# Kernel optimization log

Hardware: AMD Instinct MI355X
Metric: run time of the kernel (lower is better)

Reference implementation:

```python
import jax, jax.numpy as jnp
import numpy as np

B, S, D = 2, 2048, 1024
H, DH, DL, DR = 16, 64, 512, 64
DHID, N_SHARED, N_ROUTED, TOPK = 512, 2, 8, 2
EPS = 1e-6


def setup_inputs() -> dict:
    key = jax.random.key(0)
    ks = jax.random.split(key, 16)
    w = lambda k, shp: jax.random.normal(k, shp, dtype=jnp.float32) * 0.02
    return {
        "x": jax.random.normal(ks[0], (B, S, D), dtype=jnp.float32),
        "mask": jnp.tril(jnp.ones((S, S), dtype=bool)),  # causal
        "w_q": w(ks[1], (D, H * (DH + DR))),
        "w_dkv": w(ks[2], (D, DL)),
        "w_uk": w(ks[3], (DL, H * DH)),
        "w_uv": w(ks[4], (DL, H * DH)),
        "w_kr": w(ks[5], (D, DR)),
        "w_o": w(ks[6], (H * DH, D)),
        "attn_norm_w": jnp.ones((D,), jnp.float32),
        "mlp_norm_w": jnp.ones((D,), jnp.float32),
        "gate_w": w(ks[7], (D, N_ROUTED)),
        "wr_gate": w(ks[8], (N_ROUTED, D, DHID)),
        "wr_up": w(ks[9], (N_ROUTED, D, DHID)),
        "wr_down": w(ks[10], (N_ROUTED, DHID, D)),
        "ws_gate": w(ks[11], (N_SHARED, D, DHID)),
        "ws_up": w(ks[12], (N_SHARED, D, DHID)),
        "ws_down": w(ks[13], (N_SHARED, DHID, D)),
    }


def _rmsnorm(x, w):
    x32 = x.astype(jnp.float32)
    n = x32 * jax.lax.rsqrt(jnp.mean(x32 * x32, axis=-1, keepdims=True) + EPS)
    return n.astype(x.dtype) * w


def _rope_tables(seq_len, dim):
    half = dim // 2
    inv = 1.0 / (10000.0 ** (jnp.arange(half, dtype=jnp.float32) / half))
    ang = jnp.arange(seq_len, dtype=jnp.float32)[:, None] * inv[None, :]  # [S, dim/2]
    return jnp.cos(ang), jnp.sin(ang)


def _rope(t, cos, sin):
    # t: [..., S, dim]; rotate-half convention
    t1, t2 = jnp.split(t, 2, axis=-1)
    return jnp.concatenate([t1 * cos - t2 * sin, t2 * cos + t1 * sin], axis=-1)


def _layer(x, mask, w_q, w_dkv, w_uk, w_uv, w_kr, w_o, attn_norm_w, mlp_norm_w,
           gate_w, wr_gate, wr_up, wr_down, ws_gate, ws_up, ws_down):
    # ---- pre-norm MLA attention + residual ----
    h = _rmsnorm(x, attn_norm_w)
    cos, sin = _rope_tables(S, DR)

    q = (h @ w_q).reshape(B, S, H, DH + DR).transpose(0, 2, 1, 3)  # [B,H,S,DH+DR]
    q_c, q_r = q[..., :DH], _rope(q[..., DH:], cos, sin)

    latent = h @ w_dkv                                              # [B,S,DL]
    k_c = (latent @ w_uk).reshape(B, S, H, DH).transpose(0, 2, 1, 3)  # [B,H,S,DH]
    v = (latent @ w_uv).reshape(B, S, H, DH).transpose(0, 2, 1, 3)
    k_r = _rope(h @ w_kr, cos, sin)                                 # [B,S,DR] shared across heads

    scale = 1.0 / np.sqrt(DH + DR)
    scores = (jnp.einsum("bhqd,bhkd->bhqk", q_c, k_c)
              + jnp.einsum("bhqd,bkd->bhqk", q_r, k_r)) * scale
    scores = jnp.where(mask, scores, jnp.float32(-1e9))
    attn = jax.nn.softmax(scores, axis=-1)
    ctx = jnp.einsum("bhqk,bhkd->bhqd", attn, v)                    # [B,H,S,DH]
    attn_out = ctx.transpose(0, 2, 1, 3).reshape(B, S, H * DH) @ w_o
    x = x + attn_out

    # ---- pre-norm shared + routed MoE FFN + residual ----
    h = _rmsnorm(x, mlp_norm_w).reshape(-1, D)                      # [T,D]
    probs = jax.nn.softmax(h @ gate_w, axis=-1)                     # [T,NR]
    vals, idx = jax.lax.top_k(probs, TOPK)                          # [T,K]
    gw = vals / jnp.sum(vals, axis=-1, keepdims=True)
    dense_w = jnp.sum(jax.nn.one_hot(idx, N_ROUTED, dtype=h.dtype) * gw[..., None], axis=1)  # [T,NR]

    g = jax.nn.silu(jnp.einsum("td,edh->teh", h, wr_gate))
    u = jnp.einsum("td,edh->teh", h, wr_up)
    y = jnp.einsum("teh,ehd->ted", g * u, wr_down)                  # [T,NR,D]
    routed = jnp.einsum("ted,te->td", y, dense_w)

    gs = jax.nn.silu(jnp.einsum("td,sdh->tsh", h, ws_gate))
    us = jnp.einsum("td,sdh->tsh", h, ws_up)
    shared = jnp.einsum("tsh,shd->td", gs * us, ws_down)

    return x + (routed + shared).reshape(B, S, D)


def reference(x, mask, w_q, w_dkv, w_uk, w_uv, w_kr, w_o, attn_norm_w, mlp_norm_w,
              gate_w, wr_gate, wr_up, wr_down, ws_gate, ws_up, ws_down):
    return _layer(x, mask, w_q, w_dkv, w_uk, w_uv, w_kr, w_o, attn_norm_w, mlp_norm_w,
                  gate_w, wr_gate, wr_up, wr_down, ws_gate, ws_up, ws_down)
```

## Files before the change

### kernel.cpp

```cpp
#include <hip/hip_runtime.h>
#include <hip/hip_bf16.h>
#include <stdint.h>

typedef unsigned short u16;
typedef __attribute__((ext_vector_type(8))) short short8;
typedef __attribute__((ext_vector_type(4))) float f32x4;
typedef __attribute__((ext_vector_type(4))) int i32x4;
typedef __attribute__((ext_vector_type(2))) unsigned int u32x2;

#define B_    2
#define S_    2048
#define D_    1024
#define H_    16
#define T_    (B_*S_)

static __device__ __forceinline__ float b2f(u16 h) { return __uint_as_float(((uint32_t)h) << 16); }
static __device__ __forceinline__ u16 f2b(float f) {
    uint32_t u = __float_as_uint(f);
    u += 0x7fffu + ((u >> 16) & 1u);
    return (u16)(u >> 16);
}
static __device__ __forceinline__ uint32_t pack2(float a, float b) {
    return (uint32_t)f2b(a) | ((uint32_t)f2b(b) << 16);
}
static __device__ __forceinline__ uint32_t cvtpk(float a, float b) {
    uint32_t r;
    asm("v_cvt_pk_bf16_f32 %0, %1, %2" : "=v"(r) : "v"(a), "v"(b));
    return r;
}
#define MFMA(a,b,c) __builtin_amdgcn_mfma_f32_16x16x32_bf16(a,b,c,0,0,0)

static __device__ __forceinline__ void gl2lds16(const void* g, void* l) {
    __builtin_amdgcn_global_load_lds((const __attribute__((address_space(1))) void*)g,
                                     (__attribute__((address_space(3))) void*)l, 16, 0, 0);
}

__global__ __launch_bounds__(256) void transpose_cvt(const float* __restrict__ in,
    u16* __restrict__ out, int K, int N, long inEZ, long outEZ)
{
    __shared__ float tile[32][33];
    const int e = blockIdx.z;
    const float* ip = in + (long)e * inEZ;
    u16* op = out + (long)e * outEZ;
    int n0 = blockIdx.x * 32, k0 = blockIdx.y * 32;
    int tx = threadIdx.x, ty = threadIdx.y;
#pragma unroll
    for (int i = 0; i < 4; ++i) {
        int k = k0 + ty + 8 * i, n = n0 + tx;
        tile[ty + 8 * i][tx] = (k < K && n < N) ? ip[(long)k * N + n] : 0.f;
    }
    __syncthreads();
#pragma unroll
    for (int i = 0; i < 4; ++i) {
        int n = n0 + ty + 8 * i, k = k0 + tx;
        if (n < N && k < K) op[(long)n * K + k] = f2b(tile[tx][ty + 8 * i]);
    }
}

__global__ __launch_bounds__(256) void gemm_k(const u16* __restrict__ A, long lda,
    const u16* __restrict__ Bt, long ldb, void* __restrict__ Cv, long ldc, int K,
    int mode, const float* __restrict__ resid)
{
    __shared__ u16 As[3][128 * 32];
    __shared__ u16 Bs[3][128 * 32];
    const int tid = threadIdx.x, lane = tid & 63, wave = tid >> 6;
    const int wm = (wave & 1) * 64, wn = (wave >> 1) * 64;
    const int quad = lane >> 4, rr = lane & 15, q8 = quad * 8;
    const long row0 = (long)blockIdx.y * 128, col0 = (long)blockIdx.x * 128;
    f32x4 acc[4][4];
#pragma unroll
    for (int i = 0; i < 4; ++i)
#pragma unroll
        for (int j = 0; j < 4; ++j)
#pragma unroll
            for (int c = 0; c < 4; ++c) acc[i][j][c] = 0.f;
    const int band = wave * 32;
    const u16* ga = A + (row0 + band + (lane >> 2)) * lda + (lane & 3) * 8;
    const u16* gb = Bt + (col0 + band + (lane >> 2)) * ldb + (lane & 3) * 8;
    const int lo = band * 32;
    const int nt = K >> 5;
#define STG(bi, k0s) do { \
    gl2lds16(ga + (k0s), &As[bi][lo]); \
    gl2lds16(ga + (k0s) + 16 * lda, &As[bi][lo + 512]); \
    gl2lds16(gb + (k0s), &Bs[bi][lo]); \
    gl2lds16(gb + (k0s) + 16 * ldb, &Bs[bi][lo + 512]); } while (0)
    STG(0, 0);
    STG(1, 32);
    asm volatile("s_waitcnt vmcnt(4)" ::: "memory");
    __builtin_amdgcn_s_barrier();
    int cur = 0, nx2 = 2;
    for (int t = 0; t < nt; ++t) {
        const bool more = (t + 2 < nt);
        if (more) STG(nx2, (t + 2) * 32);
        short8 af[4], bf[4];
#pragma unroll
        for (int mi = 0; mi < 4; ++mi) af[mi] = *(const short8*)&As[cur][(wm + mi * 16 + rr) * 32 + q8];
#pragma unroll
        for (int ni = 0; ni < 4; ++ni) bf[ni] = *(const short8*)&Bs[cur][(wn + ni * 16 + rr) * 32 + q8];
#pragma unroll
        for (int mi = 0; mi < 4; ++mi)
#pragma unroll
            for (int ni = 0; ni < 4; ++ni)
                acc[mi][ni] = MFMA(af[mi], bf[ni], acc[mi][ni]);
        if (more) asm volatile("s_waitcnt vmcnt(4)" ::: "memory");
        else      asm volatile("s_waitcnt vmcnt(0)" ::: "memory");
        __builtin_amdgcn_s_barrier();
        cur = (cur == 2) ? 0 : cur + 1;
        nx2 = (nx2 == 2) ? 0 : nx2 + 1;
    }
#undef STG
#pragma unroll
    for (int mi = 0; mi < 4; ++mi)
#pragma unroll
        for (int ni = 0; ni < 4; ++ni)
#pragma unroll
            for (int rg = 0; rg < 4; ++rg) {
                long r = row0 + wm + mi * 16 + quad * 4 + rg;
                long c = col0 + wn + ni * 16 + rr;
                float v = acc[mi][ni][rg];
                if (mode == 1)      ((u16*)Cv)[r * ldc + c] = f2b(v);
                else if (mode == 2) ((float*)Cv)[r * ldc + c] += v;
                else                ((float*)Cv)[r * ldc + c] = v + resid[r * 1024 + c];
            }
}

__global__ __launch_bounds__(256) void gemm_shdown(const u16* __restrict__ A,
    const u16* __restrict__ BtBase, float* __restrict__ Cv)
{
    __shared__ u16 As[3][128 * 32];
    __shared__ u16 Bs[3][128 * 32];
    const int tid = threadIdx.x, lane = tid & 63, wave = tid >> 6;
    const int wm = (wave & 1) * 64, wn = (wave >> 1) * 64;
    const int quad = lane >> 4, rr = lane & 15, q8 = quad * 8;
    const long row0 = (long)blockIdx.y * 128, col0 = (long)blockIdx.x * 128;
    f32x4 acc[4][4];
#pragma unroll
    for (int i = 0; i < 4; ++i)
#pragma unroll
        for (int j = 0; j < 4; ++j)
#pragma unroll
            for (int c = 0; c < 4; ++c) acc[i][j][c] = 0.f;
    const int band = wave * 32;
    const long arow = row0 + band + (lane >> 2);
    const long brow = col0 + band + (lane >> 2);
    const int lo = band * 32;
#define STG(bi, k0s) do { \
    const long aoff = ((k0s) < 512) ? (long)(k0s) : (long)(512 + (k0s)); \
    const long boff = ((k0s) < 512) ? (long)(k0s) : (long)(524288 - 512 + (k0s)); \
    const u16* ga = A + arow * 2048 + aoff + (lane & 3) * 8; \
    const u16* gb = BtBase + brow * 512 + boff + (lane & 3) * 8; \
    gl2lds16(ga, &As[bi][lo]); \
    gl2lds16(ga + 16 * 2048, &As[bi][lo + 512]); \
    gl2lds16(gb, &Bs[bi][lo]); \
    gl2lds16(gb + 16 * 512, &Bs[bi][lo + 512]); } while (0)
    const int nt = 32;
    STG(0, 0);
    STG(1, 32);
    asm volatile("s_waitcnt vmcnt(4)" ::: "memory");
    __builtin_amdgcn_s_barrier();
    int cur = 0, nx2 = 2;
    for (int t = 0; t < nt; ++t) {
        const bool more = (t + 2 < nt);
        if (more) STG(nx2, (t + 2) * 32);
        short8 af[4], bf[4];
#pragma unroll
        for (int mi = 0; mi < 4; ++mi) af[mi] = *(const short8*)&As[cur][(wm + mi * 16 + rr) * 32 + q8];
#pragma unroll
        for (int ni = 0; ni < 4; ++ni) bf[ni] = *(const short8*)&Bs[cur][(wn + ni * 16 + rr) * 32 + q8];
#pragma unroll
        for (int mi = 0; mi < 4; ++mi)
#pragma unroll
            for (int ni = 0; ni < 4; ++ni)
                acc[mi][ni] = MFMA(af[mi], bf[ni], acc[mi][ni]);
        if (more) asm volatile("s_waitcnt vmcnt(4)" ::: "memory");
        else      asm volatile("s_waitcnt vmcnt(0)" ::: "memory");
        __builtin_amdgcn_s_barrier();
        cur = (cur == 2) ? 0 : cur + 1;
        nx2 = (nx2 == 2) ? 0 : nx2 + 1;
    }
#undef STG
#pragma unroll
    for (int mi = 0; mi < 4; ++mi)
#pragma unroll
        for (int ni = 0; ni < 4; ++ni)
#pragma unroll
            for (int rg = 0; rg < 4; ++rg) {
                long r = row0 + wm + mi * 16 + quad * 4 + rg;
                long c = col0 + wn + ni * 16 + rr;
                Cv[r * 1024 + c] += acc[mi][ni][rg];
            }
}

__global__ __launch_bounds__(256) void gemm_gather(const u16* __restrict__ H2,
    const u16* __restrict__ BtAll, u16* __restrict__ C,
    const int* __restrict__ cnt, const int* __restrict__ off,
    const int* __restrict__ elist)
{
    const int e = blockIdx.z;
    const int cntE = cnt[e], offE = off[e];
    const int m0 = blockIdx.y * 128;
    if (m0 >= cntE) return;
    const u16* Bt = BtAll + (long)e * 1024 * 1024;
    __shared__ u16 As[3][128 * 32];
    __shared__ u16 Bs[3][128 * 32];
    const int tid = threadIdx.x, lane = tid & 63, wave = tid >> 6;
    const int wm = (wave & 1) * 64, wn = (wave >> 1) * 64;
    const int quad = lane >> 4, rr = lane & 15, q8 = quad * 8;
    const long col0 = (long)blockIdx.x * 128;
    f32x4 acc[4][4];
#pragma unroll
    for (int i = 0; i < 4; ++i)
#pragma unroll
        for (int j = 0; j < 4; ++j)
#pragma unroll
            for (int c = 0; c < 4; ++c) acc[i][j][c] = 0.f;
    const int band = wave * 32;
    int r0 = m0 + band + (lane >> 2);
    int r1 = r0 + 16;
    int tok0 = elist[offE + (r0 < cntE ? r0 : cntE - 1)];
    int tok1 = elist[offE + (r1 < cntE ? r1 : cntE - 1)];
    const u16* ga0 = H2 + (long)tok0 * 1024 + (lane & 3) * 8;
    const u16* ga1 = H2 + (long)tok1 * 1024 + (lane & 3) * 8;
    const u16* gb = Bt + (col0 + band + (lane >> 2)) * 1024L + (lane & 3) * 8;
    const int lo = band * 32;
#define STG(bi, k0s) do { \
    gl2lds16(ga0 + (k0s), &As[bi][lo]); \
    gl2lds16(ga1 + (k0s), &As[bi][lo + 512]); \
    gl2lds16(gb + (k0s), &Bs[bi][lo]); \
    gl2lds16(gb + (k0s) + 16 * 1024, &Bs[bi][lo + 512]); } while (0)
    const int nt = 32;
    STG(0, 0);
    STG(1, 32);
    asm volatile("s_waitcnt vmcnt(4)" ::: "memory");
    __builtin_amdgcn_s_barrier();
    int cur = 0, nx2 = 2;
    for (int t = 0; t < nt; ++t) {
        const bool more = (t + 2 < nt);
        if (more) STG(nx2, (t + 2) * 32);
        short8 af[4], bf[4];
#pragma unroll
        for (int mi = 0; mi < 4; ++mi) af[mi] = *(const short8*)&As[cur][(wm + mi * 16 + rr) * 32 + q8];
#pragma unroll
        for (int ni = 0; ni < 4; ++ni) bf[ni] = *(const short8*)&Bs[cur][(wn + ni * 16 + rr) * 32 + q8];
#pragma unroll
        for (int mi = 0; mi < 4; ++mi)
#pragma unroll
            for (int ni = 0; ni < 4; ++ni)
                acc[mi][ni] = MFMA(af[mi], bf[ni], acc[mi][ni]);
        if (more) asm volatile("s_waitcnt vmcnt(4)" ::: "memory");
        else      asm volatile("s_waitcnt vmcnt(0)" ::: "memory");
        __builtin_amdgcn_s_barrier();
        cur = (cur == 2) ? 0 : cur + 1;
        nx2 = (nx2 == 2) ? 0 : nx2 + 1;
    }
#undef STG
#pragma unroll
    for (int mi = 0; mi < 4; ++mi)
#pragma unroll
        for (int ni = 0; ni < 4; ++ni)
#pragma unroll
            for (int rg = 0; rg < 4; ++rg) {
                int ml = wm + mi * 16 + quad * 4 + rg;
                long c = col0 + wn + ni * 16 + rr;
                if (m0 + ml < cntE)
                    C[(long)(offE + m0 + ml) * 1024 + c] = f2b(acc[mi][ni][rg]);
            }
}

__global__ __launch_bounds__(256) void gemm_slot(const u16* __restrict__ Act,
    const u16* __restrict__ BtAll, u16* __restrict__ rout,
    const int* __restrict__ cnt, const int* __restrict__ off)
{
    const int e = blockIdx.z;
    const int cntE = cnt[e], offE = off[e];
    const int m0 = blockIdx.y * 128;
    if (m0 >= cntE) return;
    const u16* Bt = BtAll + (long)e * 1024 * 512;
    __shared__ u16 As[3][128 * 32];
    __shared__ u16 Bs[3][128 * 32];
    const int tid = threadIdx.x, lane = tid & 63, wave = tid >> 6;
    const int wm = (wave & 1) * 64, wn = (wave >> 1) * 64;
    const int quad = lane >> 4, rr = lane & 15, q8 = quad * 8;
    const long col0 = (long)blockIdx.x * 128;
    f32x4 acc[4][4];
#pragma unroll
    for (int i = 0; i < 4; ++i)
#pragma unroll
        for (int j = 0; j < 4; ++j)
#pragma unroll
            for (int c = 0; c < 4; ++c) acc[i][j][c] = 0.f;
    const int band = wave * 32;
    int r0 = offE + m0 + band + (lane >> 2); if (r0 > 8191) r0 = 8191;
    int r1 = r0 + 16; if (r1 > 8191) r1 = 8191;
    const u16* ga0 = Act + (long)r0 * 1024 + (lane & 3) * 8;
    const u16* ga1 = Act + (long)r1 * 1024 + (lane & 3) * 8;
    const u16* gb = Bt + (col0 + band + (lane >> 2)) * 512L + (lane & 3) * 8;
    const int lo = band * 32;
#define STG(bi, k0s) do { \
    gl2lds16(ga0 + (k0s), &As[bi][lo]); \
    gl2lds16(ga1 + (k0s), &As[bi][lo + 512]); \
    gl2lds16(gb + (k0s), &Bs[bi][lo]); \
    gl2lds16(gb + (k0s) + 16 * 512, &Bs[bi][lo + 512]); } while (0)
    const int nt = 16;
    STG(0, 0);
    STG(1, 32);
    asm volatile("s_waitcnt vmcnt(4)" ::: "memory");
    __builtin_amdgcn_s_barrier();
    int cur = 0, nx2 = 2;
    for (int t = 0; t < nt; ++t) {
        const bool more = (t + 2 < nt);
        if (more) STG(nx2, (t + 2) * 32);
        short8 af[4], bf[4];
#pragma unroll
        for (int mi = 0; mi < 4; ++mi) af[mi] = *(const short8*)&As[cur][(wm + mi * 16 + rr) * 32 + q8];
#pragma unroll
        for (int ni = 0; ni < 4; ++ni) bf[ni] = *(const short8*)&Bs[cur][(wn + ni * 16 + rr) * 32 + q8];
#pragma unroll
        for (int mi = 0; mi < 4; ++mi)
#pragma unroll
            for (int ni = 0; ni < 4; ++ni)
                acc[mi][ni] = MFMA(af[mi], bf[ni], acc[mi][ni]);
        if (more) asm volatile("s_waitcnt vmcnt(4)" ::: "memory");
        else      asm volatile("s_waitcnt vmcnt(0)" ::: "memory");
        __builtin_amdgcn_s_barrier();
        cur = (cur == 2) ? 0 : cur + 1;
        nx2 = (nx2 == 2) ? 0 : nx2 + 1;
    }
#undef STG
#pragma unroll
    for (int mi = 0; mi < 4; ++mi)
#pragma unroll
        for (int ni = 0; ni < 4; ++ni)
#pragma unroll
            for (int rg = 0; rg < 4; ++rg) {
                int ml = wm + mi * 16 + quad * 4 + rg;
                long c = col0 + wn + ni * 16 + rr;
                if (m0 + ml < cntE)
                    rout[(long)(offE + m0 + ml) * 1024 + c] = f2b(acc[mi][ni][rg]);
            }
}

__global__ __launch_bounds__(256) void rmsnorm_wave(const float* __restrict__ x,
    const float* __restrict__ w, u16* __restrict__ out)
{
    const int t = blockIdx.x * 4 + (threadIdx.x >> 6);
    const int lane = threadIdx.x & 63;
    const float* xp = x + (size_t)t * D_;
    f32x4 v[4];
    float s = 0.f;
#pragma unroll
    for (int i = 0; i < 4; ++i) {
        v[i] = *(const f32x4*)&xp[lane * 4 + i * 256];
#pragma unroll
        for (int j = 0; j < 4; ++j) s += v[i][j] * v[i][j];
    }
#pragma unroll
    for (int o = 32; o > 0; o >>= 1) s += __shfl_xor(s, o);
    const float inv = rsqrtf(s * (1.f / D_) + 1e-6f);
    u16* op = out + (size_t)t * D_;
#pragma unroll
    for (int i = 0; i < 4; ++i) {
        const int d = lane * 4 + i * 256;
        f32x4 wv = *(const f32x4*)&w[d];
        u32x2 pk;
        pk[0] = pack2(v[i][0] * inv * wv[0], v[i][1] * inv * wv[1]);
        pk[1] = pack2(v[i][2] * inv * wv[2], v[i][3] * inv * wv[3]);
        *(u32x2*)&op[d] = pk;
    }
}

__global__ __launch_bounds__(256) void rmsnorm_gate_fused(const float* __restrict__ xm,
    const float* __restrict__ nw, const float* __restrict__ gw, u16* __restrict__ h2,
    int* __restrict__ tok_e, float* __restrict__ tok_w)
{
    const int t = blockIdx.x * 4 + (threadIdx.x >> 6);
    const int lane = threadIdx.x & 63;
    const float* xp = xm + (size_t)t * D_;
    f32x4 v[4];
    float s = 0.f;
#pragma unroll
    for (int i = 0; i < 4; ++i) {
        v[i] = *(const f32x4*)&xp[lane * 4 + i * 256];
#pragma unroll
        for (int j = 0; j < 4; ++j) s += v[i][j] * v[i][j];
    }
#pragma unroll
    for (int o = 32; o > 0; o >>= 1) s += __shfl_xor(s, o);
    const float inv = rsqrtf(s * (1.f / D_) + 1e-6f);
    u16* op = h2 + (size_t)t * D_;
    float part[8] = {0,0,0,0,0,0,0,0};
#pragma unroll
    for (int i = 0; i < 4; ++i) {
        const int d = lane * 4 + i * 256;
        f32x4 wv = *(const f32x4*)&nw[d];
        float hv[4];
#pragma unroll
        for (int j = 0; j < 4; ++j) hv[j] = v[i][j] * inv * wv[j];
        u32x2 pk;
        pk[0] = pack2(hv[0], hv[1]);
        pk[1] = pack2(hv[2], hv[3]);
        *(u32x2*)&op[d] = pk;
#pragma unroll
        for (int j = 0; j < 4; ++j) {
            const float* gp = gw + (size_t)(d + j) * 8;
#pragma unroll
            for (int e = 0; e < 8; ++e) part[e] += hv[j] * gp[e];
        }
    }
#pragma unroll
    for (int e = 0; e < 8; ++e)
#pragma unroll
        for (int o = 32; o > 0; o >>= 1) part[e] += __shfl_xor(part[e], o);
    if (lane == 0) {
        float mx = part[0];
#pragma unroll
        for (int e = 1; e < 8; ++e) mx = fmaxf(mx, part[e]);
        float p[8];
#pragma unroll
        for (int e = 0; e < 8; ++e) p[e] = __expf(part[e] - mx);
        int i0 = 0;
#pragma unroll
        for (int e = 1; e < 8; ++e) if (p[e] > p[i0]) i0 = e;
        int i1 = (i0 == 0) ? 1 : 0;
#pragma unroll
        for (int e = 0; e < 8; ++e) { if (e == i0) continue; if (p[e] > p[i1]) i1 = e; }
        float sw = p[i0] + p[i1];
        tok_e[2 * t] = i0;  tok_e[2 * t + 1] = i1;
        tok_w[2 * t] = p[i0] / sw;  tok_w[2 * t + 1] = p[i1] / sw;
    }
}

__global__ __launch_bounds__(256) void moe_route(const int* __restrict__ tok_e,
    int* __restrict__ cnt, int* __restrict__ off,
    int* __restrict__ elist, int* __restrict__ tslot)
{
    const int E = blockIdx.x;
    const int tid = threadIdx.x, lane = tid & 63, wave = tid >> 6;
    int ev[32];
#pragma unroll
    for (int i = 0; i < 8; ++i)
        *(i32x4*)&ev[i * 4] = *(const i32x4*)&tok_e[tid * 32 + i * 4];
    int c8[8] = {0,0,0,0,0,0,0,0};
#pragma unroll
    for (int k = 0; k < 32; ++k) ++c8[ev[k] & 7];
    int incl[8];
#pragma unroll
    for (int e = 0; e < 8; ++e) {
        int vv = c8[e];
#pragma unroll
        for (int d = 1; d < 64; d <<= 1) {
            int tmp = __shfl_up(vv, d);
            if (lane >= d) vv += tmp;
        }
        incl[e] = vv;
    }
    __shared__ int wtot[4][8];
    if (lane == 63)
#pragma unroll
        for (int e = 0; e < 8; ++e) wtot[wave][e] = incl[e];
    __syncthreads();
    int tot[8];
#pragma unroll
    for (int e = 0; e < 8; ++e) tot[e] = wtot[0][e] + wtot[1][e] + wtot[2][e] + wtot[3][e];
    int waveoff = 0;
    for (int w = 0; w < 4; ++w) if (w < wave) waveoff += wtot[w][E];
    int offE = 0;
#pragma unroll
    for (int e = 0; e < 8; ++e) if (e < E) offE += tot[e];
    int rank = offE + waveoff + (incl[E] - c8[E]);
#pragma unroll
    for (int k = 0; k < 32; ++k) {
        if ((ev[k] & 7) == E) {
            int p = tid * 32 + k;
            elist[rank] = p >> 1;
            tslot[p] = rank;
            ++rank;
        }
    }
    if (tid == 0) { cnt[E] = tot[E]; off[E] = offE; }
}

__global__ __launch_bounds__(256) void rope_all(u16* __restrict__ proj)
{
    int idx = blockIdx.x * 256 + threadIdx.x;
    int i = idx & 31;
    int r = idx >> 5;
    int t = r / 17, which = r - t * 17;
    int s = t & (S_ - 1);
    float inv = __expf(-(float)i * 0.28782313662425575f);
    float ang = (float)s * inv;
    float c = cosf(ang), sn = sinf(ang);
    u16* base = proj + (size_t)t * 2688 + (which < 16 ? which * 128 + 64 : 2560);
    float t1 = b2f(base[i]), t2 = b2f(base[32 + i]);
    base[i]      = f2b(t1 * c - t2 * sn);
    base[32 + i] = f2b(t2 * c + t1 * sn);
}

__global__ __launch_bounds__(256, 4) void attn_flash(const u16* __restrict__ proj,
    const u16* __restrict__ kc, const u16* __restrict__ vt, u16* __restrict__ ctx)
{
    const int qidx = blockIdx.x >> 5;
    const int qt = (qidx < 8) ? (31 - qidx) : (qidx < 16) ? (qidx - 8)
                 : (qidx < 24) ? (39 - qidx) : (qidx - 16);
    const int bh = blockIdx.x & 31;
    const int b = bh >> 4, h = bh & 15;
    const int q0 = qt * 64;
    const int tid = threadIdx.x, lane = tid & 63, wave = tid >> 6;
    const int quad = lane >> 4, rr = lane & 15, q8 = quad * 8;
    const int wm2 = wave * 16;

    __shared__ u16 Ks[64 * 128];
    __shared__ u16 Ps[64 * 64];

    const long tbase = (long)b * S_ + q0;
    short8 qf[4];
#pragma unroll
    for (int d0 = 0; d0 < 4; ++d0)
        qf[d0] = *(const short8*)&proj[(tbase + wm2 + rr) * 2688 + h * 128 + d0 * 32 + q8];

    f32x4 accO[4];
    float m_i = -3e38f, l_i = 0.f;
#pragma unroll
    for (int vi = 0; vi < 4; ++vi)
#pragma unroll
        for (int rg = 0; rg < 4; ++rg) accO[vi][rg] = 0.f;
    const float sc = 0.08838834764831845f * 1.4426950408889634f;

    const int srow0 = tid >> 3, sg = tid & 7;
    const int swz = sg ^ (srow0 & 7);
    const u16* kcp = kc   + ((long)b * S_ + srow0) * 1024 + h * 64 + sg * 8;
    const u16* krp = proj + ((long)b * S_ + srow0) * 2688 + 2560 + sg * 8;
    const u16* vbase = vt + (size_t)(h * 64 + rr) * 4096 + b * 2048 + q8;
    const int rg7 = rr & 7;
    int rdcol[4];
#pragma unroll
    for (int d0 = 0; d0 < 4; ++d0) rdcol[d0] = ((d0 * 4 + quad) ^ rg7) * 8;
    const int prcol0 = (((quad * 16) ^ (rg7 << 4)) >> 1);
    const int prcol1 = (((64 + quad * 16) ^ (rg7 << 4)) >> 1);

    const int nkt = qt + 1;
    short8 rk0 = *(const short8*)(kcp);
    short8 rk1 = *(const short8*)(kcp + 32 * 1024);
    short8 rm0 = *(const short8*)(krp);
    short8 rm1 = *(const short8*)(krp + (size_t)32 * 2688);

    for (int kt = 0; kt < nkt; ++kt) {
        const int k0 = kt * 64;
        *(short8*)&Ks[srow0 * 128 + swz * 8]             = rk0;
        *(short8*)&Ks[(srow0 + 32) * 128 + swz * 8]      = rk1;
        *(short8*)&Ks[srow0 * 128 + 64 + swz * 8]        = rm0;
        *(short8*)&Ks[(srow0 + 32) * 128 + 64 + swz * 8] = rm1;
        __syncthreads();

        const size_t k0s = (kt + 1 < nkt) ? (size_t)(k0 + 64) : 0;
        short8 nk0 = *(const short8*)(kcp + k0s * 1024);
        short8 nk1 = *(const short8*)(kcp + k0s * 1024 + 32 * 1024);
        short8 nm0 = *(const short8*)(krp + k0s * 2688);
        short8 nm1 = *(const short8*)(krp + k0s * 2688 + (size_t)32 * 2688);

        f32x4 accS[4];
#pragma unroll
        for (int ki = 0; ki < 4; ++ki)
#pragma unroll
            for (int rg = 0; rg < 4; ++rg) accS[ki][rg] = 0.f;
        __builtin_amdgcn_s_setprio(1);
#pragma unroll
        for (int d0 = 0; d0 < 4; ++d0) {
            short8 kf[4];
#pragma unroll
            for (int ki = 0; ki < 4; ++ki) kf[ki] = *(const short8*)&Ks[(ki * 16 + rr) * 128 + rdcol[d0]];
#pragma unroll
            for (int ki = 0; ki < 4; ++ki) accS[ki] = MFMA(kf[ki], qf[d0], accS[ki]);
        }
        __builtin_amdgcn_s_setprio(0);
        __syncthreads();

        short8 vf0[4], vf1[4];
#pragma unroll
        for (int vi = 0; vi < 4; ++vi) {
            vf0[vi] = *(const short8*)(vbase + (size_t)vi * 16 * 4096 + k0);
            vf1[vi] = *(const short8*)(vbase + (size_t)vi * 16 * 4096 + k0 + 32);
        }

        float mx = -3e38f;
        if (kt == qt) {
            const int qg = q0 + wm2 + rr;
#pragma unroll
            for (int ki = 0; ki < 4; ++ki)
#pragma unroll
                for (int rg = 0; rg < 4; ++rg) {
                    float w = accS[ki][rg] * sc;
                    if (k0 + ki * 16 + quad * 4 + rg > qg) w = -1e30f;
                    accS[ki][rg] = w;
                    mx = fmaxf(mx, w);
                }
        } else {
#pragma unroll
            for (int ki = 0; ki < 4; ++ki)
#pragma unroll
                for (int rg = 0; rg < 4; ++rg) {
                    float w = accS[ki][rg] * sc;
                    accS[ki][rg] = w;
                    mx = fmaxf(mx, w);
                }
        }
        mx = fmaxf(mx, __shfl_xor(mx, 16));
        mx = fmaxf(mx, __shfl_xor(mx, 32));
        if (__any(mx > m_i)) {
            float mnew = fmaxf(m_i, mx);
            float alpha = exp2f(m_i - mnew);
            m_i = mnew;
            l_i *= alpha;
#pragma unroll
            for (int vi = 0; vi < 4; ++vi)
#pragma unroll
                for (int rg = 0; rg < 4; ++rg) accO[vi][rg] *= alpha;
        }
        float ps = 0.f;
#pragma unroll
        for (int ki = 0; ki < 4; ++ki) {
            float p0 = exp2f(accS[ki][0] - m_i);
            float p1 = exp2f(accS[ki][1] - m_i);
            float p2 = exp2f(accS[ki][2] - m_i);
            float p3 = exp2f(accS[ki][3] - m_i);
            ps += (p0 + p1) + (p2 + p3);
            u32x2 pk; pk[0] = cvtpk(p0, p1); pk[1] = cvtpk(p2, p3);
            *(u32x2*)&Ps[(wm2 + rr) * 64 + ((((ki * 32 + quad * 8) ^ (rg7 << 4)) >> 1))] = pk;
        }
        ps += __shfl_xor(ps, 16);
        ps += __shfl_xor(ps, 32);
        l_i += ps;

        short8 pf0 = *(const short8*)&Ps[(wm2 + rr) * 64 + prcol0];
        short8 pf1 = *(const short8*)&Ps[(wm2 + rr) * 64 + prcol1];
        __builtin_amdgcn_s_setprio(1);
#pragma unroll
        for (int vi = 0; vi < 4; ++vi) accO[vi] = MFMA(vf0[vi], pf0, accO[vi]);
#pragma unroll
        for (int vi = 0; vi < 4; ++vi) accO[vi] = MFMA(vf1[vi], pf1, accO[vi]);
        __builtin_amdgcn_s_setprio(0);

        rk0 = nk0; rk1 = nk1; rm0 = nm0; rm1 = nm1;
    }
    {
        float linv = 1.f / l_i;
        long t = tbase + wm2 + rr;
#pragma unroll
        for (int vi = 0; vi < 4; ++vi) {
            u32x2 pk;
            pk[0] = pack2(accO[vi][0] * linv, accO[vi][1] * linv);
            pk[1] = pack2(accO[vi][2] * linv, accO[vi][3] * linv);
            *(u32x2*)&ctx[t * 1024 + h * 64 + vi * 16 + quad * 4] = pk;
        }
    }
}

__global__ __launch_bounds__(256) void silu_mul(u16* __restrict__ gu, int nPairRows)
{
    int i = blockIdx.x * 256 + threadIdx.x;
    if (i >= nPairRows * 64) return;
    int row = i >> 6, j8 = (i & 63) * 8;
    long base = (long)row * 1024;
    short8 g8 = *(const short8*)&gu[base + j8];
    short8 u8 = *(const short8*)&gu[base + 512 + j8];
    short8 r;
#pragma unroll
    for (int j = 0; j < 8; ++j) {
        float g = b2f((u16)g8[j]), u = b2f((u16)u8[j]);
        r[j] = (short)f2b(g / (1.f + __expf(-g)) * u);
    }
    *(short8*)&gu[base + j8] = r;
}

__global__ __launch_bounds__(256) void final_kernel(const float* __restrict__ xm,
    const u16* __restrict__ rout, const int* __restrict__ tok_slot,
    const float* __restrict__ tok_w, float* __restrict__ out)
{
    long i = ((long)blockIdx.x * 256 + threadIdx.x) * 4;
    int t = (int)(i >> 10), d = (int)(i & 1023);
    int s0 = tok_slot[2 * t], s1 = tok_slot[2 * t + 1];
    float w0 = tok_w[2 * t], w1 = tok_w[2 * t + 1];
    f32x4 xv = *(const f32x4*)&xm[i];
    u32x2 r0 = *(const u32x2*)&rout[(long)s0 * 1024 + d];
    u32x2 r1 = *(const u32x2*)&rout[(long)s1 * 1024 + d];
    f32x4 o;
    o[0] = xv[0] + w0 * b2f((u16)(r0[0] & 0xffffu)) + w1 * b2f((u16)(r1[0] & 0xffffu));
    o[1] = xv[1] + w0 * b2f((u16)(r0[0] >> 16))     + w1 * b2f((u16)(r1[0] >> 16));
    o[2] = xv[2] + w0 * b2f((u16)(r0[1] & 0xffffu)) + w1 * b2f((u16)(r1[1] & 0xffffu));
    o[3] = xv[3] + w0 * b2f((u16)(r0[1] >> 16))     + w1 * b2f((u16)(r1[1] >> 16));
    *(f32x4*)&out[i] = o;
}

#define OFF_XMID   0UL
#define OFF_H      16777216UL
#define OFF_PROJ   25165824UL
#define OFF_WGU    25165824UL
#define OFF_KC     47185920UL
#define OFF_WD     47185920UL
#define OFF_VT     55574528UL
#define OFF_GUR    57671680UL
#define OFF_CTX    63963136UL
#define OFF_WATT   72351744UL
#define OFF_ROUT   74448896UL
#define OFF_GUS    91226112UL
#define OFF_TOKE   108003328UL
#define OFF_TOKW   108036096UL
#define OFF_TSLOT  108068864UL
#define OFF_ELIST  108101632UL
#define OFF_META   108134400UL

extern "C" void kernel_launch(void* const* d_in, const int* in_sizes, int n_in,
                              void* d_out, int out_size, void* d_ws, size_t ws_size,
                              hipStream_t stream)
{
    const float* x       = (const float*)d_in[0];
    const float* w_q     = (const float*)d_in[2];
    const float* w_dkv   = (const float*)d_in[3];
    const float* w_uk    = (const float*)d_in[4];
    const float* w_uv    = (const float*)d_in[5];
    const float* w_kr    = (const float*)d_in[6];
    const float* w_o     = (const float*)d_in[7];
    const float* attn_nw = (const float*)d_in[8];
    const float* mlp_nw  = (const float*)d_in[9];
    const float* gate_w  = (const float*)d_in[10];
    const float* wr_gate = (const float*)d_in[11];
    const float* wr_up   = (const float*)d_in[12];
    const float* wr_down = (const float*)d_in[13];
    const float* ws_gate = (const float*)d_in[14];
    const float* ws_up   = (const float*)d_in[15];
    const float* ws_down = (const float*)d_in[16];
    float* out = (float*)d_out;

    char* W = (char*)d_ws;
    float* x_mid = (float*)(W + OFF_XMID);
    u16* h      = (u16*)(W + OFF_H);
    u16* h2     = (u16*)(W + OFF_H);
    u16* proj   = (u16*)(W + OFF_PROJ);
    u16* wgu_t  = (u16*)(W + OFF_WGU);
    u16* kc     = (u16*)(W + OFF_KC);
    u16* wd_t   = (u16*)(W + OFF_WD);
    u16* vt     = (u16*)(W + OFF_VT);
    u16* gu_r   = (u16*)(W + OFF_GUR);
    u16* ctx    = (u16*)(W + OFF_CTX);
    u16* wqkv_t = (u16*)(W + OFF_WATT);
    u16* wuk_t  = wqkv_t + 2688 * 1024;
    u16* wuv_t  = wuk_t + 1024 * 512;
    u16* wo_t   = wuv_t + 1024 * 512;
    u16* rout   = (u16*)(W + OFF_ROUT);
    u16* gu_s   = (u16*)(W + OFF_GUS);
    int*   tok_e = (int*)(W + OFF_TOKE);
    float* tok_w = (float*)(W + OFF_TOKW);
    int*   tslot = (int*)(W + OFF_TSLOT);
    int*   elist = (int*)(W + OFF_ELIST);
    int*   meta  = (int*)(W + OFF_META);
    int* cnt = meta, * off = meta + 8;

    dim3 tb(32, 8);
    transpose_cvt<<<dim3(64, 32, 1), tb, 0, stream>>>(w_q,   wqkv_t,               1024, 2048, 0, 0);
    transpose_cvt<<<dim3(16, 32, 1), tb, 0, stream>>>(w_dkv, wqkv_t + 2048 * 1024, 1024, 512,  0, 0);
    transpose_cvt<<<dim3(2,  32, 1), tb, 0, stream>>>(w_kr,  wqkv_t + 2560 * 1024, 1024, 64,   0, 0);
    transpose_cvt<<<dim3(32, 16, 1), tb, 0, stream>>>(w_uk,  wuk_t,                512,  1024, 0, 0);
    transpose_cvt<<<dim3(32, 16, 1), tb, 0, stream>>>(w_uv,  wuv_t,                512,  1024, 0, 0);
    transpose_cvt<<<dim3(32, 32, 1), tb, 0, stream>>>(w_o,   wo_t,                 1024, 1024, 0, 0);

    rmsnorm_wave<<<T_ / 4, 256, 0, stream>>>(x, attn_nw, h);
    gemm_k<<<dim3(21, 32), 256, 0, stream>>>(h, 1024, wqkv_t, 1024, proj, 2688, 1024, 1, nullptr);
    rope_all<<<(T_ * 17 * 32) / 256, 256, 0, stream>>>(proj);
    gemm_k<<<dim3(8, 32), 256, 0, stream>>>(proj + 2048, 2688, wuk_t, 512, kc, 1024, 512, 1, nullptr);
    gemm_k<<<dim3(32, 8), 256, 0, stream>>>(wuv_t, 512, proj + 2048, 2688, vt, 4096, 512, 1, nullptr);
    attn_flash<<<1024, 256, 0, stream>>>(proj, kc, vt, ctx);
    gemm_k<<<dim3(8, 32), 256, 0, stream>>>(ctx, 1024, wo_t, 1024, x_mid, 1024, 1024, 3, x);

    transpose_cvt<<<dim3(16, 32, 8), tb, 0, stream>>>(wr_gate, wgu_t,              1024, 512, 524288, 1048576);
    transpose_cvt<<<dim3(16, 32, 8), tb, 0, stream>>>(wr_up,   wgu_t + 512 * 1024, 1024, 512, 524288, 1048576);
    transpose_cvt<<<dim3(16, 32, 2), tb, 0, stream>>>(ws_gate, wgu_t + 8 * 1048576,              1024, 512, 524288, 1048576);
    transpose_cvt<<<dim3(16, 32, 2), tb, 0, stream>>>(ws_up,   wgu_t + 8 * 1048576 + 512 * 1024, 1024, 512, 524288, 1048576);
    transpose_cvt<<<dim3(32, 16, 8), tb, 0, stream>>>(wr_down, wd_t,               512, 1024, 524288, 524288);
    transpose_cvt<<<dim3(32, 16, 2), tb, 0, stream>>>(ws_down, wd_t + 8 * 524288,  512, 1024, 524288, 524288);

    rmsnorm_gate_fused<<<T_ / 4, 256, 0, stream>>>(x_mid, mlp_nw, gate_w, h2, tok_e, tok_w);
    moe_route<<<8, 256, 0, stream>>>(tok_e, cnt, off, elist, tslot);
    gemm_gather<<<dim3(8, 64, 8), 256, 0, stream>>>(h2, wgu_t, gu_r, cnt, off, elist);
    silu_mul<<<(8192 * 64) / 256, 256, 0, stream>>>(gu_r, 8192);
    gemm_slot<<<dim3(8, 64, 8), 256, 0, stream>>>(gu_r, wd_t, rout, cnt, off);
    gemm_k<<<dim3(16, 32), 256, 0, stream>>>(h2, 1024, wgu_t + 8 * 1048576, 1024, gu_s, 2048, 1024, 1, nullptr);
    silu_mul<<<(8192 * 64) / 256, 256, 0, stream>>>(gu_s, 8192);
    gemm_shdown<<<dim3(8, 32), 256, 0, stream>>>(gu_s, wd_t + 8 * 524288, x_mid);
    final_kernel<<<(T_ * D_) / 1024, 256, 0, stream>>>(x_mid, rout, tslot, tok_w, out);
}
```

Baseline: 570.8 us.

## Batch weight transposes and MoE GEMMs into fewer grouped kernel launches

Merges the ten separate weight transpose/convert launches into four grouped kernels that pick their source and destination from block indices. The two latent up-projection GEMMs run in one dual-problem launch. The routed and shared expert gate/up GEMMs, SiLU passes and down GEMMs are each combined into single launches dispatched on blockIdx.z. This cuts launch count and per-kernel tail bubbles, and lets shared and routed expert work share the GPU at the same time. In exchange the kernels gain extra branching, and the grid sizes now rely on per-expert counts never exceeding 4096 rows.

```diff
diff --git a/kernel.cpp b/kernel.cpp
--- a/kernel.cpp
+++ b/kernel.cpp
@@ -35,14 +35,9 @@
                                      (__attribute__((address_space(3))) void*)l, 16, 0, 0);
 }
 
-__global__ __launch_bounds__(256) void transpose_cvt(const float* __restrict__ in,
-    u16* __restrict__ out, int K, int N, long inEZ, long outEZ)
-{
-    __shared__ float tile[32][33];
-    const int e = blockIdx.z;
-    const float* ip = in + (long)e * inEZ;
-    u16* op = out + (long)e * outEZ;
-    int n0 = blockIdx.x * 32, k0 = blockIdx.y * 32;
+static __device__ __forceinline__ void tr_body(const float* __restrict__ ip,
+    u16* __restrict__ op, int K, int N, int k0, int n0, float (*tile)[33])
+{
     int tx = threadIdx.x, ty = threadIdx.y;
 #pragma unroll
     for (int i = 0; i < 4; ++i) {
@@ -55,6 +50,55 @@
         int n = n0 + ty + 8 * i, k = k0 + tx;
         if (n < N && k < K) op[(long)n * K + k] = f2b(tile[tx][ty + 8 * i]);
     }
+}
+
+__global__ __launch_bounds__(256) void transpose_attn_a(const float* __restrict__ wq,
+    const float* __restrict__ wdkv, const float* __restrict__ wkr, u16* __restrict__ out)
+{
+    __shared__ float tile[32][33];
+    int bx = blockIdx.x;
+    const float* in; u16* op; int N; int n0;
+    if (bx < 64)      { in = wq;   op = out;             N = 2048; n0 = bx * 32; }
+    else if (bx < 80) { in = wdkv; op = out + 2048*1024; N = 512;  n0 = (bx-64) * 32; }
+    else              { in = wkr;  op = out + 2560*1024; N = 64;   n0 = (bx-80) * 32; }
+    tr_body(in, op, 1024, N, blockIdx.y * 32, n0, tile);
+}
+
+__global__ __launch_bounds__(256) void transpose_attn_b(const float* __restrict__ wuk,
+    const float* __restrict__ wuv, const float* __restrict__ wo,
+    u16* __restrict__ uk_t, u16* __restrict__ uv_t, u16* __restrict__ wo_t)
+{
+    __shared__ float tile[32][33];
+    int by = blockIdx.y;
+    const float* in; u16* op; int K; int k0;
+    if (by < 16)      { in = wuk; op = uk_t; K = 512;  k0 = by * 32; }
+    else if (by < 32) { in = wuv; op = uv_t; K = 512;  k0 = (by-16) * 32; }
+    else              { in = wo;  op = wo_t; K = 1024; k0 = (by-32) * 32; }
+    tr_body(in, op, K, 1024, k0, blockIdx.x * 32, tile);
+}
+
+__global__ __launch_bounds__(256) void transpose_moe_gu(const float* __restrict__ wr_gate,
+    const float* __restrict__ wr_up, const float* __restrict__ ws_gate,
+    const float* __restrict__ ws_up, u16* __restrict__ wgu_t)
+{
+    __shared__ float tile[32][33];
+    int z = blockIdx.z;
+    const float* in; u16* op;
+    if (z < 8)       { in = wr_gate + (long)z * 524288;      op = wgu_t + (long)z * 1048576; }
+    else if (z < 16) { in = wr_up   + (long)(z-8) * 524288;  op = wgu_t + (long)(z-8) * 1048576 + 524288; }
+    else if (z < 18) { in = ws_gate + (long)(z-16) * 524288; op = wgu_t + (long)(z-8) * 1048576; }
+    else             { in = ws_up   + (long)(z-18) * 524288; op = wgu_t + (long)(z-10) * 1048576 + 524288; }
+    tr_body(in, op, 1024, 512, blockIdx.y * 32, blockIdx.x * 32, tile);
+}
+
+__global__ __launch_bounds__(256) void transpose_moe_down(const float* __restrict__ wr_down,
+    const float* __restrict__ ws_down, u16* __restrict__ wd_t)
+{
+    __shared__ float tile[32][33];
+    int z = blockIdx.z;
+    const float* in = (z < 8) ? wr_down + (long)z * 524288 : ws_down + (long)(z-8) * 524288;
+    u16* op = wd_t + (long)z * 524288;
+    tr_body(in, op, 512, 1024, blockIdx.y * 32, blockIdx.x * 32, tile);
 }
 
 __global__ __launch_bounds__(256) void gemm_k(const u16* __restrict__ A, long lda,
@@ -124,9 +168,15 @@
             }
 }
 
-__global__ __launch_bounds__(256) void gemm_shdown(const u16* __restrict__ A,
-    const u16* __restrict__ BtBase, float* __restrict__ Cv)
-{
+__global__ __launch_bounds__(256) void gemm_dual(
+    const u16* __restrict__ A0, long lda0, const u16* __restrict__ B0, long ldb0, u16* __restrict__ C0, long ldc0, int nx0, int ny0,
+    const u16* __restrict__ A1, long lda1, const u16* __restrict__ B1, long ldb1, u16* __restrict__ C1, long ldc1, int nx1, int ny1)
+{
+    const int z = blockIdx.z;
+    if ((int)blockIdx.x >= (z ? nx1 : nx0) || (int)blockIdx.y >= (z ? ny1 : ny0)) return;
+    const u16* A  = z ? A1 : A0;  const long lda = z ? lda1 : lda0;
+    const u16* Bt = z ? B1 : B0;  const long ldb = z ? ldb1 : ldb0;
+    u16* C = z ? C1 : C0;         const long ldc = z ? ldc1 : ldc0;
     __shared__ u16 As[3][128 * 32];
     __shared__ u16 Bs[3][128 * 32];
     const int tid = threadIdx.x, lane = tid & 63, wave = tid >> 6;
@@ -141,19 +191,15 @@
 #pragma unroll
             for (int c = 0; c < 4; ++c) acc[i][j][c] = 0.f;
     const int band = wave * 32;
-    const long arow = row0 + band + (lane >> 2);
-    const long brow = col0 + band + (lane >> 2);
+    const u16* ga = A + (row0 + band + (lane >> 2)) * lda + (lane & 3) * 8;
+    const u16* gb = Bt + (col0 + band + (lane >> 2)) * ldb + (lane & 3) * 8;
     const int lo = band * 32;
+    const int nt = 16;
 #define STG(bi, k0s) do { \
-    const long aoff = ((k0s) < 512) ? (long)(k0s) : (long)(512 + (k0s)); \
-    const long boff = ((k0s) < 512) ? (long)(k0s) : (long)(524288 - 512 + (k0s)); \
-    const u16* ga = A + arow * 2048 + aoff + (lane & 3) * 8; \
-    const u16* gb = BtBase + brow * 512 + boff + (lane & 3) * 8; \
-    gl2lds16(ga, &As[bi][lo]); \
-    gl2lds16(ga + 16 * 2048, &As[bi][lo + 512]); \
-    gl2lds16(gb, &Bs[bi][lo]); \
-    gl2lds16(gb + 16 * 512, &Bs[bi][lo + 512]); } while (0)
-    const int nt = 32;
+    gl2lds16(ga + (k0s), &As[bi][lo]); \
+    gl2lds16(ga + (k0s) + 16 * lda, &As[bi][lo + 512]); \
+    gl2lds16(gb + (k0s), &Bs[bi][lo]); \
+    gl2lds16(gb + (k0s) + 16 * ldb, &Bs[bi][lo + 512]); } while (0)
     STG(0, 0);
     STG(1, 32);
     asm volatile("s_waitcnt vmcnt(4)" ::: "memory");
@@ -187,20 +233,21 @@
             for (int rg = 0; rg < 4; ++rg) {
                 long r = row0 + wm + mi * 16 + quad * 4 + rg;
                 long c = col0 + wn + ni * 16 + rr;
-                Cv[r * 1024 + c] += acc[mi][ni][rg];
+                C[r * ldc + c] = f2b(acc[mi][ni][rg]);
             }
 }
 
-__global__ __launch_bounds__(256) void gemm_gather(const u16* __restrict__ H2,
-    const u16* __restrict__ BtAll, u16* __restrict__ C,
-    const int* __restrict__ cnt, const int* __restrict__ off,
-    const int* __restrict__ elist)
+__global__ __launch_bounds__(256) void gemm_guall(const u16* __restrict__ H2,
+    const u16* __restrict__ BtAll, u16* __restrict__ gu_r, u16* __restrict__ gu_s,
+    const int* __restrict__ cnt, const int* __restrict__ off, const int* __restrict__ elist)
 {
     const int e = blockIdx.z;
-    const int cntE = cnt[e], offE = off[e];
+    const bool sh = (e >= 8);
+    const int cntE = sh ? 4096 : cnt[e];
+    const int offE = sh ? 0 : off[e];
     const int m0 = blockIdx.y * 128;
     if (m0 >= cntE) return;
-    const u16* Bt = BtAll + (long)e * 1024 * 1024;
+    const u16* Bt = BtAll + (long)e * 1048576;
     __shared__ u16 As[3][128 * 32];
     __shared__ u16 Bs[3][128 * 32];
     const int tid = threadIdx.x, lane = tid & 63, wave = tid >> 6;
@@ -217,8 +264,12 @@
     const int band = wave * 32;
     int r0 = m0 + band + (lane >> 2);
     int r1 = r0 + 16;
-    int tok0 = elist[offE + (r0 < cntE ? r0 : cntE - 1)];
-    int tok1 = elist[offE + (r1 < cntE ? r1 : cntE - 1)];
+    int tok0, tok1;
+    if (sh) { tok0 = r0; tok1 = r1; }
+    else {
+        tok0 = elist[offE + (r0 < cntE ? r0 : cntE - 1)];
+        tok1 = elist[offE + (r1 < cntE ? r1 : cntE - 1)];
+    }
     const u16* ga0 = H2 + (long)tok0 * 1024 + (lane & 3) * 8;
     const u16* ga1 = H2 + (long)tok1 * 1024 + (lane & 3) * 8;
     const u16* gb = Bt + (col0 + band + (lane >> 2)) * 1024L + (lane & 3) * 8;
@@ -262,26 +313,28 @@
             for (int rg = 0; rg < 4; ++rg) {
                 int ml = wm + mi * 16 + quad * 4 + rg;
                 long c = col0 + wn + ni * 16 + rr;
-                if (m0 + ml < cntE)
-                    C[(long)(offE + m0 + ml) * 1024 + c] = f2b(acc[mi][ni][rg]);
+                if (m0 + ml < cntE) {
+                    float v = acc[mi][ni][rg];
+                    if (sh) gu_s[(long)(m0 + ml) * 2048 + (long)(e - 8) * 1024 + c] = f2b(v);
+                    else    gu_r[(long)(offE + m0 + ml) * 1024 + c] = f2b(v);
+                }
             }
 }
 
-__global__ __launch_bounds__(256) void gemm_slot(const u16* __restrict__ Act,
-    const u16* __restrict__ BtAll, u16* __restrict__ rout,
-    const int* __restrict__ cnt, const int* __restrict__ off)
+__global__ __launch_bounds__(256) void gemm_downall(const u16* __restrict__ gu_r,
+    const u16* __restrict__ gu_s, const u16* __restrict__ WdAll, u16* __restrict__ rout,
+    float* __restrict__ xmid, const int* __restrict__ cnt, const int* __restrict__ off)
 {
     const int e = blockIdx.z;
-    const int cntE = cnt[e], offE = off[e];
-    const int m0 = blockIdx.y * 128;
-    if (m0 >= cntE) return;
-    const u16* Bt = BtAll + (long)e * 1024 * 512;
     __shared__ u16 As[3][128 * 32];
     __shared__ u16 Bs[3][128 * 32];
     const int tid = threadIdx.x, lane = tid & 63, wave = tid >> 6;
     const int wm = (wave & 1) * 64, wn = (wave >> 1) * 64;
     const int quad = lane >> 4, rr = lane & 15, q8 = quad * 8;
     const long col0 = (long)blockIdx.x * 128;
+    const int m0 = blockIdx.y * 128;
+    const int band = wave * 32;
+    const int lo = band * 32;
     f32x4 acc[4][4];
 #pragma unroll
     for (int i = 0; i < 4; ++i)
@@ -289,55 +342,107 @@
         for (int j = 0; j < 4; ++j)
 #pragma unroll
             for (int c = 0; c < 4; ++c) acc[i][j][c] = 0.f;
-    const int band = wave * 32;
-    int r0 = offE + m0 + band + (lane >> 2); if (r0 > 8191) r0 = 8191;
-    int r1 = r0 + 16; if (r1 > 8191) r1 = 8191;
-    const u16* ga0 = Act + (long)r0 * 1024 + (lane & 3) * 8;
-    const u16* ga1 = Act + (long)r1 * 1024 + (lane & 3) * 8;
-    const u16* gb = Bt + (col0 + band + (lane >> 2)) * 512L + (lane & 3) * 8;
-    const int lo = band * 32;
-#define STG(bi, k0s) do { \
+    if (e < 8) {
+        const int cntE = cnt[e], offE = off[e];
+        if (m0 >= cntE) return;
+        const u16* Bt = WdAll + (long)e * 524288;
+        int r0 = offE + m0 + band + (lane >> 2); if (r0 > 8191) r0 = 8191;
+        int r1 = r0 + 16; if (r1 > 8191) r1 = 8191;
+        const u16* ga0 = gu_r + (long)r0 * 1024 + (lane & 3) * 8;
+        const u16* ga1 = gu_r + (long)r1 * 1024 + (lane & 3) * 8;
+        const u16* gb = Bt + (col0 + band + (lane >> 2)) * 512L + (lane & 3) * 8;
+#define STGR(bi, k0s) do { \
     gl2lds16(ga0 + (k0s), &As[bi][lo]); \
     gl2lds16(ga1 + (k0s), &As[bi][lo + 512]); \
     gl2lds16(gb + (k0s), &Bs[bi][lo]); \
     gl2lds16(gb + (k0s) + 16 * 512, &Bs[bi][lo + 512]); } while (0)
-    const int nt = 16;
-    STG(0, 0);
-    STG(1, 32);
-    asm volatile("s_waitcnt vmcnt(4)" ::: "memory");
-    __builtin_amdgcn_s_barrier();
-    int cur = 0, nx2 = 2;
-    for (int t = 0; t < nt; ++t) {
-        const bool more = (t + 2 < nt);
-        if (more) STG(nx2, (t + 2) * 32);
-        short8 af[4], bf[4];
-#pragma unroll
-        for (int mi = 0; mi < 4; ++mi) af[mi] = *(const short8*)&As[cur][(wm + mi * 16 + rr) * 32 + q8];
-#pragma unroll
-        for (int ni = 0; ni < 4; ++ni) bf[ni] = *(const short8*)&Bs[cur][(wn + ni * 16 + rr) * 32 + q8];
+        const int nt = 16;
+        STGR(0, 0);
+        STGR(1, 32);
+        asm volatile("s_waitcnt vmcnt(4)" ::: "memory");
+        __builtin_amdgcn_s_barrier();
+        int cur = 0, nx2 = 2;
+        for (int t = 0; t < nt; ++t) {
+            const bool more = (t + 2 < nt);
+            if (more) STGR(nx2, (t + 2) * 32);
+            short8 af[4], bf[4];
+#pragma unroll
+            for (int mi = 0; mi < 4; ++mi) af[mi] = *(const short8*)&As[cur][(wm + mi * 16 + rr) * 32 + q8];
+#pragma unroll
+            for (int ni = 0; ni < 4; ++ni) bf[ni] = *(const short8*)&Bs[cur][(wn + ni * 16 + rr) * 32 + q8];
+#pragma unroll
+            for (int mi = 0; mi < 4; ++mi)
+#pragma unroll
+                for (int ni = 0; ni < 4; ++ni)
+                    acc[mi][ni] = MFMA(af[mi], bf[ni], acc[mi][ni]);
+            if (more) asm volatile("s_waitcnt vmcnt(4)" ::: "memory");
+            else      asm volatile("s_waitcnt vmcnt(0)" ::: "memory");
+            __builtin_amdgcn_s_barrier();
+            cur = (cur == 2) ? 0 : cur + 1;
+            nx2 = (nx2 == 2) ? 0 : nx2 + 1;
+        }
+#undef STGR
 #pragma unroll
         for (int mi = 0; mi < 4; ++mi)
 #pragma unroll
             for (int ni = 0; ni < 4; ++ni)
-                acc[mi][ni] = MFMA(af[mi], bf[ni], acc[mi][ni]);
-        if (more) asm volatile("s_waitcnt vmcnt(4)" ::: "memory");
-        else      asm volatile("s_waitcnt vmcnt(0)" ::: "memory");
+#pragma unroll
+                for (int rg = 0; rg < 4; ++rg) {
+                    int ml = wm + mi * 16 + quad * 4 + rg;
+                    long c = col0 + wn + ni * 16 + rr;
+                    if (m0 + ml < cntE)
+                        rout[(long)(offE + m0 + ml) * 1024 + c] = f2b(acc[mi][ni][rg]);
+                }
+    } else {
+        const u16* BtBase = WdAll + 8L * 524288;
+        const long arow = m0 + band + (lane >> 2);
+        const long brow = col0 + band + (lane >> 2);
+#define STGS(bi, k0s) do { \
+    const long aoff = ((k0s) < 512) ? (long)(k0s) : (long)(512 + (k0s)); \
+    const long boff = ((k0s) < 512) ? (long)(k0s) : (long)(524288 - 512 + (k0s)); \
+    const u16* ga = gu_s + arow * 2048 + aoff + (lane & 3) * 8; \
+    const u16* gb = BtBase + brow * 512 + boff + (lane & 3) * 8; \
+    gl2lds16(ga, &As[bi][lo]); \
+    gl2lds16(ga + 16 * 2048, &As[bi][lo + 512]); \
+    gl2lds16(gb, &Bs[bi][lo]); \
+    gl2lds16(gb + 16 * 512, &Bs[bi][lo + 512]); } while (0)
+        const int nt = 32;
+        STGS(0, 0);
+        STGS(1, 32);
+        asm volatile("s_waitcnt vmcnt(4)" ::: "memory");
         __builtin_amdgcn_s_barrier();
-        cur = (cur == 2) ? 0 : cur + 1;
-        nx2 = (nx2 == 2) ? 0 : nx2 + 1;
-    }
-#undef STG
-#pragma unroll
-    for (int mi = 0; mi < 4; ++mi)
-#pragma unroll
-        for (int ni = 0; ni < 4; ++ni)
-#pragma unroll
-            for (int rg = 0; rg < 4; ++rg) {
-                int ml = wm + mi * 16 + quad * 4 + rg;
-                long c = col0 + wn + ni * 16 + rr;
-                if (m0 + ml < cntE)
-                    rout[(long)(offE + m0 + ml) * 1024 + c] = f2b(acc[mi][ni][rg]);
-            }
+        int cur = 0, nx2 = 2;
+        for (int t = 0; t < nt; ++t) {
+            const bool more = (t + 2 < nt);
+            if (more) STGS(nx2, (t + 2) * 32);
+            short8 af[4], bf[4];
+#pragma unroll
+            for (int mi = 0; mi < 4; ++mi) af[mi] = *(const short8*)&As[cur][(wm + mi * 16 + rr) * 32 + q8];
+#pragma unroll
+            for (int ni = 0; ni < 4; ++ni) bf[ni] = *(const short8*)&Bs[cur][(wn + ni * 16 + rr) * 32 + q8];
+#pragma unroll
+            for (int mi = 0; mi < 4; ++mi)
+#pragma unroll
+                for (int ni = 0; ni < 4; ++ni)
+                    acc[mi][ni] = MFMA(af[mi], bf[ni], acc[mi][ni]);
+            if (more) asm volatile("s_waitcnt vmcnt(4)" ::: "memory");
+            else      asm volatile("s_waitcnt vmcnt(0)" ::: "memory");
+            __builtin_amdgcn_s_barrier();
+            cur = (cur == 2) ? 0 : cur + 1;
+            nx2 = (nx2 == 2) ? 0 : nx2 + 1;
+        }
+#undef STGS
+#pragma unroll
+        for (int mi = 0; mi < 4; ++mi)
+#pragma unroll
+            for (int ni = 0; ni < 4; ++ni)
+#pragma unroll
+                for (int rg = 0; rg < 4; ++rg) {
+                    long r = m0 + wm + mi * 16 + quad * 4 + rg;
+                    long c = col0 + wn + ni * 16 + rr;
+                    xmid[r * 1024 + c] += acc[mi][ni][rg];
+                }
+    }
 }
 
 __global__ __launch_bounds__(256) void rmsnorm_wave(const float* __restrict__ x,
@@ -655,21 +760,20 @@
     }
 }
 
-__global__ __launch_bounds__(256) void silu_mul(u16* __restrict__ gu, int nPairRows)
+__global__ __launch_bounds__(256) void silu_all(u16* __restrict__ gu_r, u16* __restrict__ gu_s)
 {
     int i = blockIdx.x * 256 + threadIdx.x;
-    if (i >= nPairRows * 64) return;
     int row = i >> 6, j8 = (i & 63) * 8;
-    long base = (long)row * 1024;
-    short8 g8 = *(const short8*)&gu[base + j8];
-    short8 u8 = *(const short8*)&gu[base + 512 + j8];
+    u16* gu = (row < 8192) ? gu_r + (long)row * 1024 : gu_s + (long)(row - 8192) * 1024;
+    short8 g8 = *(const short8*)&gu[j8];
+    short8 u8 = *(const short8*)&gu[512 + j8];
     short8 r;
 #pragma unroll
     for (int j = 0; j < 8; ++j) {
         float g = b2f((u16)g8[j]), u = b2f((u16)u8[j]);
         r[j] = (short)f2b(g / (1.f + __expf(-g)) * u);
     }
-    *(short8*)&gu[base + j8] = r;
+    *(short8*)&gu[j8] = r;
 }
 
 __global__ __launch_bounds__(256) void final_kernel(const float* __restrict__ xm,
@@ -756,35 +860,25 @@
     int* cnt = meta, * off = meta + 8;
 
     dim3 tb(32, 8);
-    transpose_cvt<<<dim3(64, 32, 1), tb, 0, stream>>>(w_q,   wqkv_t,               1024, 2048, 0, 0);
-    transpose_cvt<<<dim3(16, 32, 1), tb, 0, stream>>>(w_dkv, wqkv_t + 2048 * 1024, 1024, 512,  0, 0);
-    transpose_cvt<<<dim3(2,  32, 1), tb, 0, stream>>>(w_kr,  wqkv_t + 2560 * 1024, 1024, 64,   0, 0);
-    transpose_cvt<<<dim3(32, 16, 1), tb, 0, stream>>>(w_uk,  wuk_t,                512,  1024, 0, 0);
-    transpose_cvt<<<dim3(32, 16, 1), tb, 0, stream>>>(w_uv,  wuv_t,                512,  1024, 0, 0);
-    transpose_cvt<<<dim3(32, 32, 1), tb, 0, stream>>>(w_o,   wo_t,                 1024, 1024, 0, 0);
+    transpose_attn_a<<<dim3(82, 32), tb, 0, stream>>>(w_q, w_dkv, w_kr, wqkv_t);
+    transpose_attn_b<<<dim3(32, 64), tb, 0, stream>>>(w_uk, w_uv, w_o, wuk_t, wuv_t, wo_t);
 
     rmsnorm_wave<<<T_ / 4, 256, 0, stream>>>(x, attn_nw, h);
     gemm_k<<<dim3(21, 32), 256, 0, stream>>>(h, 1024, wqkv_t, 1024, proj, 2688, 1024, 1, nullptr);
     rope_all<<<(T_ * 17 * 32) / 256, 256, 0, stream>>>(proj);
-    gemm_k<<<dim3(8, 32), 256, 0, stream>>>(proj + 2048, 2688, wuk_t, 512, kc, 1024, 512, 1, nullptr);
-    gemm_k<<<dim3(32, 8), 256, 0, stream>>>(wuv_t, 512, proj + 2048, 2688, vt, 4096, 512, 1, nullptr);
+    gemm_dual<<<dim3(32, 32, 2), 256, 0, stream>>>(
+        proj + 2048, 2688, wuk_t, 512, kc, 1024, 8, 32,
+        wuv_t, 512, proj + 2048, 2688, vt, 4096, 32, 8);
     attn_flash<<<1024, 256, 0, stream>>>(proj, kc, vt, ctx);
     gemm_k<<<dim3(8, 32), 256, 0, stream>>>(ctx, 1024, wo_t, 1024, x_mid, 1024, 1024, 3, x);
 
-    transpose_cvt<<<dim3(16, 32, 8), tb, 0, stream>>>(wr_gate, wgu_t,              1024, 512, 524288, 1048576);
-    transpose_cvt<<<dim3(16, 32, 8), tb, 0, stream>>>(wr_up,   wgu_t + 512 * 1024, 1024, 512, 524288, 1048576);
-    transpose_cvt<<<dim3(16, 32, 2), tb, 0, stream>>>(ws_gate, wgu_t + 8 * 1048576,              1024, 512, 524288, 1048576);
-    transpose_cvt<<<dim3(16, 32, 2), tb, 0, stream>>>(ws_up,   wgu_t + 8 * 1048576 + 512 * 1024, 1024, 512, 524288, 1048576);
-    transpose_cvt<<<dim3(32, 16, 8), tb, 0, stream>>>(wr_down, wd_t,               512, 1024, 524288, 524288);
-    transpose_cvt<<<dim3(32, 16, 2), tb, 0, stream>>>(ws_down, wd_t + 8 * 524288,  512, 1024, 524288, 524288);
+    transpose_moe_gu<<<dim3(16, 32, 20), tb, 0, stream>>>(wr_gate, wr_up, ws_gate, ws_up, wgu_t);
+    transpose_moe_down<<<dim3(32, 16, 10), tb, 0, stream>>>(wr_down, ws_down, wd_t);
 
     rmsnorm_gate_fused<<<T_ / 4, 256, 0, stream>>>(x_mid, mlp_nw, gate_w, h2, tok_e, tok_w);
     moe_route<<<8, 256, 0, stream>>>(tok_e, cnt, off, elist, tslot);
-    gemm_gather<<<dim3(8, 64, 8), 256, 0, stream>>>(h2, wgu_t, gu_r, cnt, off, elist);
-    silu_mul<<<(8192 * 64) / 256, 256, 0, stream>>>(gu_r, 8192);
-    gemm_slot<<<dim3(8, 64, 8), 256, 0, stream>>>(gu_r, wd_t, rout, cnt, off);
-    gemm_k<<<dim3(16, 32), 256, 0, stream>>>(h2, 1024, wgu_t + 8 * 1048576, 1024, gu_s, 2048, 1024, 1, nullptr);
-    silu_mul<<<(8192 * 64) / 256, 256, 0, stream>>>(gu_s, 8192);
-    gemm_shdown<<<dim3(8, 32), 256, 0, stream>>>(gu_s, wd_t + 8 * 524288, x_mid);
+    gemm_guall<<<dim3(8, 32, 10), 256, 0, stream>>>(h2, wgu_t, gu_r, gu_s, cnt, off, elist);
+    silu_all<<<(16384 * 64) / 256, 256, 0, stream>>>(gu_r, gu_s);
+    gemm_downall<<<dim3(8, 32, 9), 256, 0, stream>>>(gu_r, gu_s, wd_t, rout, x_mid, cnt, off);
     final_kernel<<<(T_ * D_) / 1024, 256, 0, stream>>>(x_mid, rout, tslot, tok_w, out);
 }
```

New measurement: 525.4 us. -8.0%, faster.
